# Performance work log

Hardware: AMD Instinct MI355X
Metric: run time of the kernel (lower is better)

## Reference

```python
import jax, jax.numpy as jnp
import numpy as np

D, L, H = 10000, 512, 1024
B = 8

def setup_inputs() -> dict:
    key = jax.random.key(0)
    k1, k2, k3 = jax.random.split(key, 3)
    vocab = jax.random.normal(k1, (D, H), dtype=jnp.float32)
    description = jax.random.normal(k2, (B, L, H), dtype=jnp.float32)
    default_embedding = jax.random.uniform(k3, (H,), dtype=jnp.float32)
    return {"vocab": vocab, "description": description, "default_embedding": default_embedding}

def reference(vocab, description, default_embedding):
    # full_vocab: (D+1, H) -- concept vocab plus learned default embedding
    full_vocab = jnp.concatenate([vocab, default_embedding[None, :]], axis=0)
    # logits: (B, L, D+1) = tokens @ full_vocab.T (broadcast over batch, no repeat needed)
    logits = jnp.einsum('blh,dh->bld', description, full_vocab)
    similarity = jax.nn.softmax(logits, axis=2)
    # blend: default-slot weight times raw tokens + concept-weighted vocab mix
    concept_based = similarity[:, :, -1:] * description + jnp.einsum('bld,dh->blh', similarity[:, :, :-1], vocab)
    return (concept_based, similarity)
```

## Files before the change

### kernel.cpp

```cpp
#include <hip/hip_runtime.h>
#include <stdint.h>

#define D_    10000
#define DP1   10001
#define NPAD2 10240
#define H_    1024
#define BL    4096
#define CANDS 1024
#define GC    512

typedef float  f32x4  __attribute__((ext_vector_type(4)));
typedef __bf16 bf16x8 __attribute__((ext_vector_type(8)));
typedef unsigned short u16;
typedef u16    u16x8  __attribute__((ext_vector_type(8)));

__device__ __forceinline__ u16 f2bf(float x) {
    union { float f; unsigned u; } v; v.f = x;
    unsigned r = v.u + 0x7FFFu + ((v.u >> 16) & 1u);
    return (u16)(r >> 16);
}

#define GLOAD_LDS16(gsrc, ldst)                                             \
    __builtin_amdgcn_global_load_lds(                                       \
        (__attribute__((address_space(1))) void*)(void*)(gsrc),             \
        (__attribute__((address_space(3))) void*)(void*)(ldst), 16, 0, 0)


__global__ __launch_bounds__(256)
void split_desc_k(const float* __restrict__ desc, u16* __restrict__ hi) {
    size_t i = ((size_t)blockIdx.x * 256 + threadIdx.x) * 8;
    f32x4 x0 = *(const f32x4*)(desc + i);
    f32x4 x1 = *(const f32x4*)(desc + i + 4);
    u16x8 h;
#pragma unroll
    for (int e = 0; e < 4; e++) { h[e] = f2bf(x0[e]); h[4 + e] = f2bf(x1[e]); }
    *(u16x8*)(hi + i) = h;
}

__global__ __launch_bounds__(256)
void split_fv_k(const float* __restrict__ vocab, const float* __restrict__ defe,
                u16* __restrict__ hi) {
    size_t i = ((size_t)blockIdx.x * 256 + threadIdx.x) * 8;
    int d = (int)(i >> 10);
    f32x4 x0 = {0.f, 0.f, 0.f, 0.f}, x1 = {0.f, 0.f, 0.f, 0.f};
    if (d < D_) {
        x0 = *(const f32x4*)(vocab + i);
        x1 = *(const f32x4*)(vocab + i + 4);
    } else if (d == D_) {
        int h = (int)(i & 1023);
        x0 = *(const f32x4*)(defe + h);
        x1 = *(const f32x4*)(defe + h + 4);
    }
    u16x8 h8;
#pragma unroll
    for (int e = 0; e < 4; e++) { h8[e] = f2bf(x0[e]); h8[4 + e] = f2bf(x1[e]); }
    *(u16x8*)(hi + i) = h8;
}


#define G1_MFMA(a, b, c) __builtin_amdgcn_mfma_f32_16x16x32_bf16((a), (b), (c), 0, 0, 0)

#define G1_STAGE(AhB, BhB, kk) do {                                         \
    GLOAD_LDS16(a_h  + (kk), (char*)(AhB) + tid16);                         \
    GLOAD_LDS16(b_h0 + (kk), (char*)(BhB) + tid16);                         \
    GLOAD_LDS16(b_h1 + (kk), (char*)(BhB) + tid16 + 8192);                  \
} while (0)

#define G1_ITER(AhB, BhB, t) do {                                           \
    bf16x8 afh[4], bfh[4];                                                  \
    _Pragma("unroll")                                                       \
    for (int i = 0; i < 4; i++) {                                           \
        afh[i] = *(const bf16x8*)&AhB[aoff[i]];                             \
        bfh[i] = *(const bf16x8*)&BhB[boff[i]];                             \
    }                                                                       \
    __builtin_amdgcn_s_setprio(1);                                          \
    _Pragma("unroll")                                                       \
    for (int i = 0; i < 2; i++)                                             \
        _Pragma("unroll")                                                   \
        for (int j = 0; j < 4; j++)                                         \
            acc[i][j] = G1_MFMA(afh[i], bfh[j], acc[i][j]);                 \
    __builtin_amdgcn_s_setprio(0);                                          \
    asm volatile("s_waitcnt lgkmcnt(0)" ::: "memory");                      \
    __builtin_amdgcn_s_barrier();                                           \
    if ((t) + 2 < 32) G1_STAGE(AhB, BhB, ((t) + 2) * 32);                   \
    __builtin_amdgcn_s_setprio(1);                                          \
    _Pragma("unroll")                                                       \
    for (int i = 2; i < 4; i++)                                             \
        _Pragma("unroll")                                                   \
        for (int j = 0; j < 4; j++)                                         \
            acc[i][j] = G1_MFMA(afh[i], bfh[j], acc[i][j]);                 \
    __builtin_amdgcn_s_setprio(0);                                          \
    if ((t) + 2 < 32)      asm volatile("s_waitcnt vmcnt(3)" ::: "memory"); \
    else if ((t) + 1 < 32) asm volatile("s_waitcnt vmcnt(0)" ::: "memory"); \
    __builtin_amdgcn_s_barrier();                                           \
} while (0)

__global__ __launch_bounds__(512, 2)
void gemm1_k(const u16* __restrict__ Ahg, const u16* __restrict__ Bhg,
             float* __restrict__ C) {
    __shared__ u16 Ah0[128 * 32], Bh0[256 * 32];
    __shared__ u16 Ah1[128 * 32], Bh1[256 * 32];

    const int tid  = threadIdx.x;
    const int wave = tid >> 6, lane = tid & 63;
    const int wr = wave >> 2, wc = wave & 3;
    const int quad = lane >> 4, r16 = lane & 15;
    const int m0 = blockIdx.y * 128, n0 = blockIdx.x * 256;

    f32x4 zero = {0.f, 0.f, 0.f, 0.f};
    f32x4 acc[4][4];
#pragma unroll
    for (int i = 0; i < 4; i++)
#pragma unroll
        for (int j = 0; j < 4; j++) acc[i][j] = zero;

    const int arow = tid >> 2, achk = tid & 3;
    const int ascol = (achk ^ ((arow >> 1) & 3)) * 8;
    const u16* a_h = Ahg + (size_t)(m0 + arow) * H_ + ascol;
    const int brow0 = arow,        bscol0 = (achk ^ ((brow0 >> 1) & 3)) * 8;
    const int brow1 = 128 + arow,  bscol1 = (achk ^ ((brow1 >> 1) & 3)) * 8;
    const u16* b_h0 = Bhg + (size_t)(n0 + brow0) * H_ + bscol0;
    const u16* b_h1 = Bhg + (size_t)(n0 + brow1) * H_ + bscol1;
    const int tid16 = tid * 16;
    const int aswz = (r16 >> 1) & 3;

    int aoff[4], boff[4];
#pragma unroll
    for (int i = 0; i < 4; i++) {
        aoff[i] = (wr * 64 + i * 16 + r16) * 32 + ((quad ^ aswz) * 8);
        boff[i] = (wc * 64 + i * 16 + r16) * 32 + ((quad ^ aswz) * 8);
    }

    G1_STAGE(Ah0, Bh0, 0);
    G1_STAGE(Ah1, Bh1, 32);
    asm volatile("s_waitcnt vmcnt(3)" ::: "memory");
    __builtin_amdgcn_s_barrier();

    for (int t = 0; t < 32; t += 2) {
        G1_ITER(Ah0, Bh0, t);
        G1_ITER(Ah1, Bh1, t + 1);
    }

#pragma unroll
    for (int i = 0; i < 4; i++) {
        int gm = m0 + wr * 64 + i * 16 + quad * 4;
#pragma unroll
        for (int j = 0; j < 4; j++) {
            int gn = n0 + wc * 64 + j * 16 + r16;
            if (gn < DP1) {
#pragma unroll
                for (int reg = 0; reg < 4; reg++)
                    C[(size_t)(gm + reg) * DP1 + gn] = acc[i][j][reg];
            }
        }
    }
}

__global__ __launch_bounds__(1024)
void softmax_cand_k(float* __restrict__ sim, int* __restrict__ gcnt,
                    int* __restrict__ gcidx) {
    __shared__ float red[16];
    __shared__ int   cnt;
    __shared__ int   cidx[GC];
    const int tid = threadIdx.x;
    const int row = blockIdx.x;
    float* rowp = sim + (size_t)row * DP1;
    if (tid == 0) cnt = 0;

    const int a0 = (4 - (row & 3)) & 3;
    const int b0 = a0 + tid * 4;
    const int b1 = a0 + 4096 + tid * 4;
    const int b2 = a0 + 8192 + tid * 4;

    float vh = (tid < a0) ? rowp[tid] : -3.4e38f;
    f32x4 v0 = *(const f32x4*)(rowp + b0);
    f32x4 v1 = *(const f32x4*)(rowp + b1);
    f32x4 v2;
    if (b2 + 3 <= D_) {
        v2 = *(const f32x4*)(rowp + b2);
    } else {
#pragma unroll
        for (int e = 0; e < 4; e++)
            v2[e] = (b2 + e <= D_) ? rowp[b2 + e] : -3.4e38f;
    }

    float mx = vh;
#pragma unroll
    for (int e = 0; e < 4; e++) mx = fmaxf(mx, fmaxf(v0[e], fmaxf(v1[e], v2[e])));
#pragma unroll
    for (int off = 32; off; off >>= 1) mx = fmaxf(mx, __shfl_down(mx, off, 64));
    if ((tid & 63) == 0) red[tid >> 6] = mx;
    __syncthreads();
#pragma unroll
    for (int w = 0; w < 16; w++) mx = fmaxf(mx, red[w]);

    float s0 = 0.f;
    vh = __expf(vh - mx); s0 += vh;
#pragma unroll
    for (int e = 0; e < 4; e++) {
        v0[e] = __expf(v0[e] - mx); s0 += v0[e];
        v1[e] = __expf(v1[e] - mx); s0 += v1[e];
        v2[e] = __expf(v2[e] - mx); s0 += v2[e];
    }
#pragma unroll
    for (int off = 32; off; off >>= 1) s0 += __shfl_down(s0, off, 64);
    __syncthreads();
    if ((tid & 63) == 0) red[tid >> 6] = s0;
    __syncthreads();
    float sum = 0.f;
#pragma unroll
    for (int w = 0; w < 16; w++) sum += red[w];
    const float inv = 1.f / sum;
    const float thr = sum * 1e-8f;

    if (tid < a0) {
        float p = vh * inv;
        rowp[tid] = p;
        if (vh > thr) {
            int k = atomicAdd(&cnt, 1);
            if (k < GC) cidx[k] = tid;
        }
    }
    {
        f32x4 p0 = v0 * inv;
        *(f32x4*)(rowp + b0) = p0;
#pragma unroll
        for (int e = 0; e < 4; e++)
            if (v0[e] > thr) {
                int k = atomicAdd(&cnt, 1);
                if (k < GC) cidx[k] = b0 + e;
            }
        f32x4 p1 = v1 * inv;
        *(f32x4*)(rowp + b1) = p1;
#pragma unroll
        for (int e = 0; e < 4; e++)
            if (v1[e] > thr) {
                int k = atomicAdd(&cnt, 1);
                if (k < GC) cidx[k] = b1 + e;
            }
#pragma unroll
        for (int e = 0; e < 4; e++) {
            int idx = b2 + e;
            if (idx <= D_) {
                float p = v2[e] * inv;
                rowp[idx] = p;
                if (idx < D_ && v2[e] > thr) {
                    int k = atomicAdd(&cnt, 1);
                    if (k < GC) cidx[k] = idx;
                }
            }
        }
    }
    __syncthreads();

    const int k = cnt < GC ? cnt : GC;
    if (tid < k) gcidx[(size_t)row * GC + tid] = cidx[tid];
    if (tid == 0) gcnt[row] = cnt;
}

__global__ __launch_bounds__(256)
void gather_k(float* __restrict__ sim, const int* __restrict__ gcnt,
              const int* __restrict__ gcidx,
              const float* __restrict__ vocab, const float* __restrict__ defe,
              const float* __restrict__ desc, float* __restrict__ out) {
    __shared__ float lex[GC + 1];
    __shared__ float psh[GC + 1];
    const int tid = threadIdx.x;
    const int row = blockIdx.x;
    const int cnt0 = gcnt[row];
    const int cnt = cnt0 < GC ? cnt0 : GC;
    const float* drow = desc + (size_t)row * H_;
    const int lane = tid & 63, wv = tid >> 6;
    const int* crow = gcidx + (size_t)row * GC;

    for (int c = wv; c <= cnt; c += 4) {
        const float* vrow = (c == cnt) ? defe : (vocab + (size_t)crow[c] * H_);
        float s = 0.f;
#pragma unroll
        for (int q = 0; q < 4; q++) {
            f32x4 dv = *(const f32x4*)(drow + (q * 64 + lane) * 4);
            f32x4 vv = *(const f32x4*)(vrow + (q * 64 + lane) * 4);
            s += dv[0] * vv[0] + dv[1] * vv[1] + dv[2] * vv[2] + dv[3] * vv[3];
        }
#pragma unroll
        for (int off = 32; off; off >>= 1) s += __shfl_down(s, off, 64);
        if (lane == 0) lex[c] = s;
    }
    __syncthreads();

    float m = -3.4e38f;
    for (int c = 0; c <= cnt; c++) m = fmaxf(m, lex[c]);
    float Z = 0.f;
    for (int c = 0; c <= cnt; c++) Z += __expf(lex[c] - m);
    const float invZ = 1.f / Z;
    for (int i = tid; i <= cnt; i += 256) psh[i] = __expf(lex[i] - m) * invZ;
    __syncthreads();

    float* rowp = sim + (size_t)row * DP1;
    for (int c = tid; c < cnt; c += 256) rowp[crow[c]] = psh[c];
    if (tid == 0) rowp[D_] = psh[cnt];

    f32x4 a = psh[cnt] * ((const f32x4*)drow)[tid];
    if (cnt0 <= GC) {
        for (int c = 0; c < cnt; c++)
            a += psh[c] * ((const f32x4*)(vocab + (size_t)crow[c] * H_))[tid];
    } else {
        for (int d = 0; d < D_; d++) {
            float p = rowp[d];
            if (p > 1e-8f) a += p * ((const f32x4*)(vocab + (size_t)d * H_))[tid];
        }
    }
    ((f32x4*)(out + (size_t)row * H_))[tid] = a;
}

__global__ __launch_bounds__(256)
void naive_logits_k(const float* __restrict__ vocab, const float* __restrict__ desc,
                    const float* __restrict__ defe, float* __restrict__ sim) {
    int d = blockIdx.x * 256 + threadIdx.x;
    if (d >= DP1) return;
    const float* vr = (d < D_) ? (vocab + (size_t)d * H_) : defe;
    const float* dr = desc + (size_t)blockIdx.y * H_;
    float s = 0.f;
    for (int h = 0; h < H_; h++) s = fmaf(dr[h], vr[h], s);
    sim[(size_t)blockIdx.y * DP1 + d] = s;
}

__global__ __launch_bounds__(1024)
void softmax_gather_k(float* __restrict__ sim, const float* __restrict__ vocab,
                      const float* __restrict__ desc, float* __restrict__ out) {
    __shared__ float red[16];
    __shared__ float wslot;
    __shared__ int   cnt;
    __shared__ int   cidx[CANDS];
    __shared__ float cp[CANDS];
    const int tid = threadIdx.x;
    const int row = blockIdx.x;
    float* rowp = sim + (size_t)row * DP1;
    if (tid == 0) cnt = 0;

    const int a0 = (4 - (row & 3)) & 3;
    const int b0 = a0 + tid * 4;
    const int b1 = a0 + 4096 + tid * 4;
    const int b2 = a0 + 8192 + tid * 4;

    float vh = (tid < a0) ? rowp[tid] : -3.4e38f;
    f32x4 v0 = *(const f32x4*)(rowp + b0);
    f32x4 v1 = *(const f32x4*)(rowp + b1);
    f32x4 v2;
    if (b2 + 3 <= D_) {
        v2 = *(const f32x4*)(rowp + b2);
    } else {
#pragma unroll
        for (int e = 0; e < 4; e++)
            v2[e] = (b2 + e <= D_) ? rowp[b2 + e] : -3.4e38f;
    }

    float mx = vh;
#pragma unroll
    for (int e = 0; e < 4; e++) mx = fmaxf(mx, fmaxf(v0[e], fmaxf(v1[e], v2[e])));
#pragma unroll
    for (int off = 32; off; off >>= 1) mx = fmaxf(mx, __shfl_down(mx, off, 64));
    if ((tid & 63) == 0) red[tid >> 6] = mx;
    __syncthreads();
#pragma unroll
    for (int w = 0; w < 16; w++) mx = fmaxf(mx, red[w]);

    float s0 = 0.f;
    vh = __expf(vh - mx); s0 += vh;
#pragma unroll
    for (int e = 0; e < 4; e++) {
        v0[e] = __expf(v0[e] - mx); s0 += v0[e];
        v1[e] = __expf(v1[e] - mx); s0 += v1[e];
        v2[e] = __expf(v2[e] - mx); s0 += v2[e];
    }
#pragma unroll
    for (int off = 32; off; off >>= 1) s0 += __shfl_down(s0, off, 64);
    __syncthreads();
    if ((tid & 63) == 0) red[tid >> 6] = s0;
    __syncthreads();
    float sum = 0.f;
#pragma unroll
    for (int w = 0; w < 16; w++) sum += red[w];
    const float inv = 1.f / sum;
    const float thr = sum * 1e-7f;

    if (tid < a0) {
        float p = vh * inv;
        rowp[tid] = p;
        if (vh > thr) {
            int k = atomicAdd(&cnt, 1);
            if (k < CANDS) { cidx[k] = tid; cp[k] = p; }
        }
    }
    {
        f32x4 p0 = v0 * inv;
        *(f32x4*)(rowp + b0) = p0;
#pragma unroll
        for (int e = 0; e < 4; e++)
            if (v0[e] > thr) {
                int k = atomicAdd(&cnt, 1);
                if (k < CANDS) { cidx[k] = b0 + e; cp[k] = p0[e]; }
            }
        f32x4 p1 = v1 * inv;
        *(f32x4*)(rowp + b1) = p1;
#pragma unroll
        for (int e = 0; e < 4; e++)
            if (v1[e] > thr) {
                int k = atomicAdd(&cnt, 1);
                if (k < CANDS) { cidx[k] = b1 + e; cp[k] = p1[e]; }
            }
#pragma unroll
        for (int e = 0; e < 4; e++) {
            int idx = b2 + e;
            if (idx <= D_) {
                float p = v2[e] * inv;
                rowp[idx] = p;
                if (idx == D_) wslot = p;
                else if (v2[e] > thr) {
                    int k = atomicAdd(&cnt, 1);
                    if (k < CANDS) { cidx[k] = idx; cp[k] = p; }
                }
            }
        }
    }
    __syncthreads();

    const float w = wslot;
    float a = w * desc[(size_t)row * H_ + tid];
    if (cnt <= CANDS) {
        const int k = cnt;
        for (int c = 0; c < k; c++)
            a += cp[c] * vocab[(size_t)cidx[c] * H_ + tid];
    } else {
        const float pthr = thr * inv;
        for (int d = 0; d < D_; d++) {
            float p = rowp[d];
            if (p > pthr) a += p * vocab[(size_t)d * H_ + tid];
        }
    }
    out[(size_t)row * H_ + tid] = a;
}

extern "C" void kernel_launch(void* const* d_in, const int* in_sizes, int n_in,
                              void* d_out, int out_size, void* d_ws, size_t ws_size,
                              hipStream_t stream) {
    (void)in_sizes; (void)n_in; (void)out_size;
    const float* vocab = (const float*)d_in[0];
    const float* desc  = (const float*)d_in[1];
    const float* defe  = (const float*)d_in[2];
    float* out = (float*)d_out;
    float* sim = out + (size_t)BL * H_;

    const size_t REQ1 = 29360128ull;
    char* ws = (char*)d_ws;

    if (ws_size >= REQ1) {
        u16* dhi = (u16*)(ws + 0);
        u16* fhi = (u16*)(ws + 8388608);

        split_desc_k<<<2048, 256, 0, stream>>>(desc, dhi);
        split_fv_k<<<5120, 256, 0, stream>>>(vocab, defe, fhi);
        gemm1_k<<<dim3(40, 32), 512, 0, stream>>>(dhi, fhi, sim);

        int* gcnt  = (int*)(ws + 0);
        int* gcidx = (int*)(ws + 32768);
        softmax_cand_k<<<4096, 1024, 0, stream>>>(sim, gcnt, gcidx);
        gather_k<<<4096, 256, 0, stream>>>(sim, gcnt, gcidx, vocab, defe, desc, out);
    } else {
        naive_logits_k<<<dim3(40, BL), 256, 0, stream>>>(vocab, desc, defe, sim);
        softmax_gather_k<<<4096, 1024, 0, stream>>>(sim, vocab, desc, out);
    }
}
```

Baseline: 389.2 us.

## Store bf16 logits to workspace and fuse softmax, candidate refinement and gather

The GEMM now writes its logits as bf16 into a padded workspace buffer instead of writing fp32 logits into the similarity output. The softmax, candidate selection, fp32 rescoring of candidates and the weighted vocab gather are merged into one kernel per row, so fp32 logits no longer make a round trip through the output and the candidate lists no longer go through global memory. The cost is a larger workspace requirement that could trigger the naive fallback path. The final similarity write also does a per-element linear search over the candidate list, and the output gather switches from float4 to scalar loads.

```diff
diff --git a/kernel.cpp b/kernel.cpp
--- a/kernel.cpp
+++ b/kernel.cpp
@@ -4,6 +4,7 @@
 #define D_    10000
 #define DP1   10001
 #define NPAD2 10240
+#define LGW   10240
 #define H_    1024
 #define BL    4096
 #define CANDS 1024
@@ -18,6 +19,10 @@
     union { float f; unsigned u; } v; v.f = x;
     unsigned r = v.u + 0x7FFFu + ((v.u >> 16) & 1u);
     return (u16)(r >> 16);
+}
+__device__ __forceinline__ float bf2f(u16 b) {
+    union { float f; unsigned u; } v; v.u = ((unsigned)b) << 16;
+    return v.f;
 }
 
 #define GLOAD_LDS16(gsrc, ldst)                                             \
@@ -97,7 +102,7 @@
 
 __global__ __launch_bounds__(512, 2)
 void gemm1_k(const u16* __restrict__ Ahg, const u16* __restrict__ Bhg,
-             float* __restrict__ C) {
+             u16* __restrict__ Lg) {
     __shared__ u16 Ah0[128 * 32], Bh0[256 * 32];
     __shared__ u16 Ah1[128 * 32], Bh1[256 * 32];
 
@@ -147,170 +152,164 @@
 #pragma unroll
         for (int j = 0; j < 4; j++) {
             int gn = n0 + wc * 64 + j * 16 + r16;
-            if (gn < DP1) {
-#pragma unroll
-                for (int reg = 0; reg < 4; reg++)
-                    C[(size_t)(gm + reg) * DP1 + gn] = acc[i][j][reg];
-            }
+#pragma unroll
+            for (int reg = 0; reg < 4; reg++)
+                Lg[(size_t)(gm + reg) * LGW + gn] = f2bf(acc[i][j][reg]);
         }
     }
 }
 
 __global__ __launch_bounds__(1024)
-void softmax_cand_k(float* __restrict__ sim, int* __restrict__ gcnt,
-                    int* __restrict__ gcidx) {
+void softmax_finish_k(const u16* __restrict__ Lg, float* __restrict__ sim,
+                      const float* __restrict__ vocab, const float* __restrict__ defe,
+                      const float* __restrict__ desc, float* __restrict__ out) {
     __shared__ float red[16];
     __shared__ int   cnt;
     __shared__ int   cidx[GC];
-    const int tid = threadIdx.x;
-    const int row = blockIdx.x;
-    float* rowp = sim + (size_t)row * DP1;
-    if (tid == 0) cnt = 0;
-
-    const int a0 = (4 - (row & 3)) & 3;
-    const int b0 = a0 + tid * 4;
-    const int b1 = a0 + 4096 + tid * 4;
-    const int b2 = a0 + 8192 + tid * 4;
-
-    float vh = (tid < a0) ? rowp[tid] : -3.4e38f;
-    f32x4 v0 = *(const f32x4*)(rowp + b0);
-    f32x4 v1 = *(const f32x4*)(rowp + b1);
-    f32x4 v2;
-    if (b2 + 3 <= D_) {
-        v2 = *(const f32x4*)(rowp + b2);
-    } else {
-#pragma unroll
-        for (int e = 0; e < 4; e++)
-            v2[e] = (b2 + e <= D_) ? rowp[b2 + e] : -3.4e38f;
-    }
-
-    float mx = vh;
-#pragma unroll
-    for (int e = 0; e < 4; e++) mx = fmaxf(mx, fmaxf(v0[e], fmaxf(v1[e], v2[e])));
-#pragma unroll
-    for (int off = 32; off; off >>= 1) mx = fmaxf(mx, __shfl_down(mx, off, 64));
-    if ((tid & 63) == 0) red[tid >> 6] = mx;
-    __syncthreads();
-#pragma unroll
-    for (int w = 0; w < 16; w++) mx = fmaxf(mx, red[w]);
-
-    float s0 = 0.f;
-    vh = __expf(vh - mx); s0 += vh;
-#pragma unroll
-    for (int e = 0; e < 4; e++) {
-        v0[e] = __expf(v0[e] - mx); s0 += v0[e];
-        v1[e] = __expf(v1[e] - mx); s0 += v1[e];
-        v2[e] = __expf(v2[e] - mx); s0 += v2[e];
-    }
-#pragma unroll
-    for (int off = 32; off; off >>= 1) s0 += __shfl_down(s0, off, 64);
-    __syncthreads();
-    if ((tid & 63) == 0) red[tid >> 6] = s0;
-    __syncthreads();
-    float sum = 0.f;
-#pragma unroll
-    for (int w = 0; w < 16; w++) sum += red[w];
-    const float inv = 1.f / sum;
-    const float thr = sum * 1e-8f;
-
-    if (tid < a0) {
-        float p = vh * inv;
-        rowp[tid] = p;
-        if (vh > thr) {
-            int k = atomicAdd(&cnt, 1);
-            if (k < GC) cidx[k] = tid;
-        }
-    }
-    {
-        f32x4 p0 = v0 * inv;
-        *(f32x4*)(rowp + b0) = p0;
-#pragma unroll
-        for (int e = 0; e < 4; e++)
-            if (v0[e] > thr) {
-                int k = atomicAdd(&cnt, 1);
-                if (k < GC) cidx[k] = b0 + e;
-            }
-        f32x4 p1 = v1 * inv;
-        *(f32x4*)(rowp + b1) = p1;
-#pragma unroll
-        for (int e = 0; e < 4; e++)
-            if (v1[e] > thr) {
-                int k = atomicAdd(&cnt, 1);
-                if (k < GC) cidx[k] = b1 + e;
-            }
-#pragma unroll
-        for (int e = 0; e < 4; e++) {
-            int idx = b2 + e;
-            if (idx <= D_) {
-                float p = v2[e] * inv;
-                rowp[idx] = p;
-                if (idx < D_ && v2[e] > thr) {
-                    int k = atomicAdd(&cnt, 1);
-                    if (k < GC) cidx[k] = idx;
-                }
-            }
-        }
-    }
-    __syncthreads();
-
-    const int k = cnt < GC ? cnt : GC;
-    if (tid < k) gcidx[(size_t)row * GC + tid] = cidx[tid];
-    if (tid == 0) gcnt[row] = cnt;
-}
-
-__global__ __launch_bounds__(256)
-void gather_k(float* __restrict__ sim, const int* __restrict__ gcnt,
-              const int* __restrict__ gcidx,
-              const float* __restrict__ vocab, const float* __restrict__ defe,
-              const float* __restrict__ desc, float* __restrict__ out) {
     __shared__ float lex[GC + 1];
     __shared__ float psh[GC + 1];
     const int tid = threadIdx.x;
     const int row = blockIdx.x;
-    const int cnt0 = gcnt[row];
-    const int cnt = cnt0 < GC ? cnt0 : GC;
+    const u16* lrow = Lg + (size_t)row * LGW;
+    float* rowp = sim + (size_t)row * DP1;
     const float* drow = desc + (size_t)row * H_;
+    if (tid == 0) cnt = 0;
+
+    const int iA = tid * 8;
+    const int iB = 8192 + tid * 8;
+    float va[8], vb[8];
+    {
+        u16x8 ra = *(const u16x8*)(lrow + iA);
+#pragma unroll
+        for (int e = 0; e < 8; e++) va[e] = bf2f(ra[e]);
+    }
+    if (tid < 256) {
+        u16x8 rb = *(const u16x8*)(lrow + iB);
+#pragma unroll
+        for (int e = 0; e < 8; e++) vb[e] = (iB + e <= D_) ? bf2f(rb[e]) : -3.4e38f;
+    } else {
+#pragma unroll
+        for (int e = 0; e < 8; e++) vb[e] = -3.4e38f;
+    }
+
+    float mx = -3.4e38f;
+#pragma unroll
+    for (int e = 0; e < 8; e++) mx = fmaxf(mx, fmaxf(va[e], vb[e]));
+#pragma unroll
+    for (int off = 32; off; off >>= 1) mx = fmaxf(mx, __shfl_down(mx, off, 64));
+    if ((tid & 63) == 0) red[tid >> 6] = mx;
+    __syncthreads();
+#pragma unroll
+    for (int w = 0; w < 16; w++) mx = fmaxf(mx, red[w]);
+
+    float s0 = 0.f;
+#pragma unroll
+    for (int e = 0; e < 8; e++) {
+        va[e] = __expf(va[e] - mx); s0 += va[e];
+        vb[e] = __expf(vb[e] - mx); s0 += vb[e];
+    }
+#pragma unroll
+    for (int off = 32; off; off >>= 1) s0 += __shfl_down(s0, off, 64);
+    __syncthreads();
+    if ((tid & 63) == 0) red[tid >> 6] = s0;
+    __syncthreads();
+    float sum = 0.f;
+#pragma unroll
+    for (int w = 0; w < 16; w++) sum += red[w];
+    const float inv = 1.f / sum;
+    const float thr = sum * 1e-8f;
+
+#pragma unroll
+    for (int e = 0; e < 8; e++)
+        if (va[e] > thr) {
+            int k = atomicAdd(&cnt, 1);
+            if (k < GC) cidx[k] = iA + e;
+        }
+    if (tid < 256) {
+#pragma unroll
+        for (int e = 0; e < 8; e++) {
+            int idx = iB + e;
+            if (idx < D_ && vb[e] > thr) {
+                int k = atomicAdd(&cnt, 1);
+                if (k < GC) cidx[k] = idx;
+            }
+        }
+    }
+    __syncthreads();
+
+    const int cnt0 = cnt;
+    const bool ovf = cnt0 > GC;
+    const int cc = ovf ? GC : cnt0;
     const int lane = tid & 63, wv = tid >> 6;
-    const int* crow = gcidx + (size_t)row * GC;
-
-    for (int c = wv; c <= cnt; c += 4) {
-        const float* vrow = (c == cnt) ? defe : (vocab + (size_t)crow[c] * H_);
-        float s = 0.f;
-#pragma unroll
-        for (int q = 0; q < 4; q++) {
-            f32x4 dv = *(const f32x4*)(drow + (q * 64 + lane) * 4);
-            f32x4 vv = *(const f32x4*)(vrow + (q * 64 + lane) * 4);
-            s += dv[0] * vv[0] + dv[1] * vv[1] + dv[2] * vv[2] + dv[3] * vv[3];
-        }
-#pragma unroll
-        for (int off = 32; off; off >>= 1) s += __shfl_down(s, off, 64);
-        if (lane == 0) lex[c] = s;
-    }
-    __syncthreads();
-
-    float m = -3.4e38f;
-    for (int c = 0; c <= cnt; c++) m = fmaxf(m, lex[c]);
-    float Z = 0.f;
-    for (int c = 0; c <= cnt; c++) Z += __expf(lex[c] - m);
-    const float invZ = 1.f / Z;
-    for (int i = tid; i <= cnt; i += 256) psh[i] = __expf(lex[i] - m) * invZ;
-    __syncthreads();
-
-    float* rowp = sim + (size_t)row * DP1;
-    for (int c = tid; c < cnt; c += 256) rowp[crow[c]] = psh[c];
-    if (tid == 0) rowp[D_] = psh[cnt];
-
-    f32x4 a = psh[cnt] * ((const f32x4*)drow)[tid];
-    if (cnt0 <= GC) {
-        for (int c = 0; c < cnt; c++)
-            a += psh[c] * ((const f32x4*)(vocab + (size_t)crow[c] * H_))[tid];
+
+    if (!ovf) {
+        for (int c = wv; c <= cc; c += 16) {
+            const float* vrow = (c == cc) ? defe : (vocab + (size_t)cidx[c] * H_);
+            float s = 0.f;
+#pragma unroll
+            for (int q = 0; q < 4; q++) {
+                f32x4 dv = *(const f32x4*)(drow + (q * 64 + lane) * 4);
+                f32x4 vv = *(const f32x4*)(vrow + (q * 64 + lane) * 4);
+                s += dv[0] * vv[0] + dv[1] * vv[1] + dv[2] * vv[2] + dv[3] * vv[3];
+            }
+#pragma unroll
+            for (int off = 32; off; off >>= 1) s += __shfl_down(s, off, 64);
+            if (lane == 0) lex[c] = s;
+        }
+        __syncthreads();
+        float m = -3.4e38f;
+        for (int c = 0; c <= cc; c++) m = fmaxf(m, lex[c]);
+        float Z = 0.f;
+        for (int c = 0; c <= cc; c++) Z += __expf(lex[c] - m);
+        const float invZ = 1.f / Z;
+        for (int i = tid; i <= cc; i += 1024) psh[i] = __expf(lex[i] - m) * invZ;
+        __syncthreads();
+    }
+
+    {
+        f32x4 p0, p1;
+#pragma unroll
+        for (int e = 0; e < 8; e++) {
+            float p = va[e] * inv;
+            if (!ovf && va[e] > thr) {
+                for (int c = 0; c < cc; c++)
+                    if (cidx[c] == iA + e) { p = psh[c]; break; }
+            }
+            if (e < 4) p0[e] = p; else p1[e - 4] = p;
+        }
+        *(f32x4*)(rowp + iA) = p0;
+        *(f32x4*)(rowp + iA + 4) = p1;
+    }
+    if (tid < 256) {
+#pragma unroll
+        for (int e = 0; e < 8; e++) {
+            int idx = iB + e;
+            if (idx <= D_) {
+                float p = vb[e] * inv;
+                if (idx == D_) { if (!ovf) p = psh[cc]; }
+                else if (!ovf && vb[e] > thr) {
+                    for (int c = 0; c < cc; c++)
+                        if (cidx[c] == idx) { p = psh[c]; break; }
+                }
+                rowp[idx] = p;
+            }
+        }
+    }
+
+    float a;
+    if (!ovf) {
+        a = psh[cc] * drow[tid];
+        for (int c = 0; c < cc; c++)
+            a += psh[c] * vocab[(size_t)cidx[c] * H_ + tid];
     } else {
+        __syncthreads();
+        a = rowp[D_] * drow[tid];
         for (int d = 0; d < D_; d++) {
             float p = rowp[d];
-            if (p > 1e-8f) a += p * ((const f32x4*)(vocab + (size_t)d * H_))[tid];
-        }
-    }
-    ((f32x4*)(out + (size_t)row * H_))[tid] = a;
+            if (p > 1e-8f) a += p * vocab[(size_t)d * H_ + tid];
+        }
+    }
+    out[(size_t)row * H_ + tid] = a;
 }
 
 __global__ __launch_bounds__(256)
@@ -451,21 +450,18 @@
     float* out = (float*)d_out;
     float* sim = out + (size_t)BL * H_;
 
-    const size_t REQ1 = 29360128ull;
+    const size_t REQ = 113246208ull;
     char* ws = (char*)d_ws;
 
-    if (ws_size >= REQ1) {
+    if (ws_size >= REQ) {
         u16* dhi = (u16*)(ws + 0);
         u16* fhi = (u16*)(ws + 8388608);
+        u16* Lg  = (u16*)(ws + 29360128);
 
         split_desc_k<<<2048, 256, 0, stream>>>(desc, dhi);
         split_fv_k<<<5120, 256, 0, stream>>>(vocab, defe, fhi);
-        gemm1_k<<<dim3(40, 32), 512, 0, stream>>>(dhi, fhi, sim);
-
-        int* gcnt  = (int*)(ws + 0);
-        int* gcidx = (int*)(ws + 32768);
-        softmax_cand_k<<<4096, 1024, 0, stream>>>(sim, gcnt, gcidx);
-        gather_k<<<4096, 256, 0, stream>>>(sim, gcnt, gcidx, vocab, defe, desc, out);
+        gemm1_k<<<dim3(40, 32), 512, 0, stream>>>(dhi, fhi, Lg);
+        softmax_finish_k<<<4096, 1024, 0, stream>>>(Lg, sim, vocab, defe, desc, out);
     } else {
         naive_logits_k<<<dim3(40, BL), 256, 0, stream>>>(vocab, desc, defe, sim);
         softmax_gather_k<<<4096, 1024, 0, stream>>>(sim, vocab, desc, out);
```

After: 434.3 us. +11.6%, slower.
